# Kernel optimization log

Hardware: AMD Instinct MI355X
Metric: run time of the kernel (lower is better)

Reference implementation:

```python
import jax, jax.numpy as jnp
import numpy as np

NUM_HEADS = 8
NUM_GROUPS = 32
EPS = 1e-5


def setup_inputs() -> dict:
    key = jax.random.key(0)
    ks = jax.random.split(key, 7)
    B, C, H, W = 16, 512, 32, 32
    x = jax.random.normal(ks[0], (B, C, H, W), dtype=jnp.float32)
    gn_gamma = jnp.ones((C,), dtype=jnp.float32)
    gn_beta = jnp.zeros((C,), dtype=jnp.float32)
    # Conv1d with kernel_size=1 is a per-position matmul: weight [out, in]
    qkv_w = jax.random.normal(ks[1], (3 * C, C), dtype=jnp.float32) / np.sqrt(C)
    qkv_b = jax.random.normal(ks[2], (3 * C,), dtype=jnp.float32) * 0.01
    proj_w = jax.random.normal(ks[3], (C, C), dtype=jnp.float32) / np.sqrt(C)
    proj_b = jax.random.normal(ks[4], (C,), dtype=jnp.float32) * 0.01
    return {"x": x, "gn_gamma": gn_gamma, "gn_beta": gn_beta,
            "qkv_w": qkv_w, "qkv_b": qkv_b, "proj_w": proj_w, "proj_b": proj_b}


def group_norm(x, gamma, beta):
    # x: [B, C, H, W]
    B, C, H, W = x.shape
    xg = x.reshape(B, NUM_GROUPS, C // NUM_GROUPS, H, W)
    mean = xg.mean(axis=(2, 3, 4), keepdims=True)
    var = xg.var(axis=(2, 3, 4), keepdims=True)
    xg = (xg - mean) * jax.lax.rsqrt(var + EPS)
    x = xg.reshape(B, C, H, W)
    return x * gamma[None, :, None, None] + beta[None, :, None, None]


def reference(x, gn_gamma, gn_beta, qkv_w, qkv_b, proj_w, proj_b):
    B, C, H, W = x.shape
    N = H * W
    hd = C // NUM_HEADS  # head dim
    h = group_norm(x, gn_gamma, gn_beta).reshape(B, C, N)
    # 1x1 Conv1d == matmul over channel dim
    qkv = jnp.einsum('oc,bcn->bon', qkv_w, h) + qkv_b[None, :, None]
    qkv = qkv.reshape(B, 3, NUM_HEADS, hd, N)
    q, k, v = qkv[:, 0], qkv[:, 1], qkv[:, 2]  # each [B, h, d, N]
    scale = hd ** (-0.5)
    attn = jnp.einsum('bhdn,bhdm->bhnm', q, k) * scale  # [B, h, N, N]
    attn = jax.nn.softmax(attn, axis=-1)
    out = jnp.einsum('bhnm,bhdm->bhdn', attn, v).reshape(B, C, N)
    out = jnp.einsum('oc,bcn->bon', proj_w, out) + proj_b[None, :, None]
    return x + out.reshape(B, C, H, W)
```

## Files before the change

### kernel.cpp

```cpp
#include <hip/hip_runtime.h>

typedef unsigned short u16;
typedef unsigned int u32;
typedef __bf16 bf16x8 __attribute__((ext_vector_type(8)));
typedef float f32x4 __attribute__((ext_vector_type(4)));
typedef float f32x16 __attribute__((ext_vector_type(16)));

#define B_ 16
#define C_ 512
#define N_ 1024
#define NB_ 16384
#define K_ 512
#define M3_ 1536
#define SCALE_Q 0.18033688011112042f

__device__ __forceinline__ u16 f2bf(float f) {
  u32 u = __float_as_uint(f);
  u32 r = (u + 0x7FFFu + ((u >> 16) & 1u)) >> 16;
  return (u16)r;
}

__device__ __forceinline__ void gl_lds16(const void* g, void* l) {
  __builtin_amdgcn_global_load_lds(
      (const __attribute__((address_space(1))) u32*)(uintptr_t)g,
      (__attribute__((address_space(3))) u32*)(u32)(uintptr_t)l, 16, 0, 0);
}

__device__ __forceinline__ u32 cvtpk(float lo, float hi) {
  u32 r;
  asm("v_cvt_pk_bf16_f32 %0, %1, %2" : "=v"(r) : "v"(lo), "v"(hi));
  return r;
}

__device__ __forceinline__ float exp2a(float x) {
  float r;
  asm("v_exp_f32 %0, %1" : "=v"(r) : "v"(x));
  return r;
}

__device__ __forceinline__ void plswap2(u32& a, u32& b) {
#if __has_builtin(__builtin_amdgcn_permlane32_swap)
  auto r = __builtin_amdgcn_permlane32_swap((int)a, (int)b, false, false);
  a = (u32)r[0];
  b = (u32)r[1];
#else
  asm("v_permlane32_swap_b32 %0, %1" : "+v"(a), "+v"(b));
#endif
}

__device__ __forceinline__ float xhalf_sum(float x) {
  u32 a = __float_as_uint(x), b = a;
  plswap2(a, b);
  return __uint_as_float(a) + __uint_as_float(b);
}

__global__ __launch_bounds__(256) void cast_bf16_kernel(const float* __restrict__ src,
                                                        u16* __restrict__ dst, int n) {
  int i = blockIdx.x * 256 + threadIdx.x;
  if (i < n) dst[i] = f2bf(src[i]);
}

__global__ __launch_bounds__(256) void gnorm_kernel(const float* __restrict__ x,
                                                    const float* __restrict__ gamma,
                                                    const float* __restrict__ beta,
                                                    u16* __restrict__ ht) {
  int blk = blockIdx.x;
  int b = blk >> 5, g = blk & 31;
  int t = threadIdx.x;
  const float* xb = x + ((size_t)(b * C_ + g * 16) << 10);
  float v[16][4];
  float s = 0.f, sq = 0.f;
#pragma unroll
  for (int cc = 0; cc < 16; ++cc) {
#pragma unroll
    for (int r = 0; r < 4; ++r) {
      float f = xb[cc * 1024 + r * 256 + t];
      v[cc][r] = f; s += f; sq += f * f;
    }
  }
#pragma unroll
  for (int m = 32; m >= 1; m >>= 1) { s += __shfl_xor(s, m, 64); sq += __shfl_xor(sq, m, 64); }
  __shared__ float red[8];
  int w = t >> 6;
  if ((t & 63) == 0) { red[w * 2] = s; red[w * 2 + 1] = sq; }
  __syncthreads();
  s = red[0] + red[2] + red[4] + red[6];
  sq = red[1] + red[3] + red[5] + red[7];
  float mean = s * (1.f / 16384.f);
  float var = sq * (1.f / 16384.f) - mean * mean;
  float rstd = rsqrtf(var + 1e-5f);
  float gm[16], bt[16];
#pragma unroll
  for (int cc = 0; cc < 16; ++cc) {
    gm[cc] = gamma[g * 16 + cc] * rstd;
    bt[cc] = beta[g * 16 + cc];
  }
  u16* hb = ht + ((size_t)(b << 10)) * C_ + g * 16;
#pragma unroll
  for (int r = 0; r < 4; ++r) {
    u32 pk[8];
#pragma unroll
    for (int q = 0; q < 8; ++q) {
      float f0 = (v[2 * q][r] - mean) * gm[2 * q] + bt[2 * q];
      float f1 = (v[2 * q + 1][r] - mean) * gm[2 * q + 1] + bt[2 * q + 1];
      pk[q] = (u32)f2bf(f0) | ((u32)f2bf(f1) << 16);
    }
    u16* dp = hb + (size_t)(r * 256 + t) * C_;
    uint4 a = {pk[0], pk[1], pk[2], pk[3]};
    uint4 b4 = {pk[4], pk[5], pk[6], pk[7]};
    *(uint4*)dp = a;
    *(uint4*)(dp + 8) = b4;
  }
}

template <int EPI>
__global__ __launch_bounds__(256) void gemm_kernel(const u16* __restrict__ A,
                                                   const u16* __restrict__ BT,
                                                   const float* __restrict__ bias,
                                                   u16* __restrict__ Co,
                                                   u16* __restrict__ qTo,
                                                   u16* __restrict__ kTo,
                                                   const float* __restrict__ xres,
                                                   float* __restrict__ Fo) {
  __shared__ u16 ldsA[128 * 64];
  __shared__ u16 ldsB[128 * 64];
  int t = threadIdx.x;
  int l = t & 63, w = t >> 6;
  int wr = w >> 1, wc = w & 1;
  int ro0 = blockIdx.y * 128, co0 = blockIdx.x * 128;
  f32x4 acc[4][4];
#pragma unroll
  for (int m = 0; m < 4; ++m)
#pragma unroll
    for (int n = 0; n < 4; ++n) acc[m][n] = {0.f, 0.f, 0.f, 0.f};
  int srow = t >> 3, sg = t & 7;
  for (int kt = 0; kt < 8; ++kt) {
    int k0 = kt * 64;
#pragma unroll
    for (int i = 0; i < 4; ++i) {
      int row = i * 32 + srow;
      int gl = sg ^ (row & 7);
      gl_lds16(A + (size_t)(ro0 + row) * K_ + k0 + gl * 8, ldsA + (i * 32 + w * 8) * 64);
      gl_lds16(BT + (size_t)(co0 + row) * K_ + k0 + gl * 8, ldsB + (i * 32 + w * 8) * 64);
    }
    __syncthreads();
#pragma unroll
    for (int ks = 0; ks < 2; ++ks) {
      bf16x8 af[4], bfr[4];
#pragma unroll
      for (int m = 0; m < 4; ++m) {
        int row = wr * 64 + m * 16 + (l & 15);
        int ph = (ks * 4 + (l >> 4)) ^ (row & 7);
        af[m] = *(const bf16x8*)&ldsA[row * 64 + ph * 8];
      }
#pragma unroll
      for (int n = 0; n < 4; ++n) {
        int row = wc * 64 + n * 16 + (l & 15);
        int ph = (ks * 4 + (l >> 4)) ^ (row & 7);
        bfr[n] = *(const bf16x8*)&ldsB[row * 64 + ph * 8];
      }
#pragma unroll
      for (int m = 0; m < 4; ++m)
#pragma unroll
        for (int n = 0; n < 4; ++n)
          acc[m][n] = __builtin_amdgcn_mfma_f32_16x16x32_bf16(af[m], bfr[n], acc[m][n], 0, 0, 0);
    }
    __syncthreads();
  }
  if (EPI == 0 && ro0 < 1024) {
    int sel = ro0 >> 9;
    u16* dstb = sel ? kTo : qTo;
    float scl = sel ? 1.f : SCALE_Q;
#pragma unroll
    for (int m = 0; m < 4; ++m) {
      int row0 = ro0 + wr * 64 + m * 16 + (l >> 4) * 4;
      int o = row0 & 511;
      int h = o >> 6, d0 = o & 63;
      float bv0 = bias[row0], bv1 = bias[row0 + 1];
      float bv2 = bias[row0 + 2], bv3 = bias[row0 + 3];
#pragma unroll
      for (int n = 0; n < 4; ++n) {
        int col = co0 + wc * 64 + n * 16 + (l & 15);
        int bb = col >> 10, nn = col & 1023;
        float v0 = (acc[m][n][0] + bv0) * scl;
        float v1 = (acc[m][n][1] + bv1) * scl;
        float v2 = (acc[m][n][2] + bv2) * scl;
        float v3 = (acc[m][n][3] + bv3) * scl;
        uint2 ov = {cvtpk(v0, v1), cvtpk(v2, v3)};
        *(uint2*)(dstb + ((size_t)((bb * 8 + h) << 10) + nn) * 64 + d0) = ov;
      }
    }
  } else {
#pragma unroll
    for (int m = 0; m < 4; ++m) {
#pragma unroll
      for (int j = 0; j < 4; ++j) {
        int row = ro0 + wr * 64 + m * 16 + (l >> 4) * 4 + j;
        float bv = bias[row];
#pragma unroll
        for (int n = 0; n < 4; ++n) {
          int col = co0 + wc * 64 + n * 16 + (l & 15);
          float val = acc[m][n][j] + bv;
          if (EPI == 0) {
            Co[(size_t)row * NB_ + col] = f2bf(val);
          } else {
            int bb = col >> 10, nn = col & 1023;
            size_t oi = (((size_t)(bb * C_ + row)) << 10) + nn;
            Fo[oi] = xres[oi] + val;
          }
        }
      }
    }
  }
}

__global__ __launch_bounds__(128) void attn_kernel(const u16* __restrict__ qT,
                                                   const u16* __restrict__ kT,
                                                   const u16* __restrict__ qkv,
                                                   u16* __restrict__ aoT) {
  __shared__ u16 Kall[2][2][2048];
  __shared__ u16 Vall[2][2][2048];
  int bid = blockIdx.x;
  int wid = (bid & 7) * 128 + (bid >> 3);
  int qt2 = wid & 7, h = (wid >> 3) & 7, b = wid >> 6;
  int bh = b * 8 + h;
  int t = threadIdx.x, l = t & 63, w = t >> 6;
  int lq = l & 31, hi = l >> 5;
  int q0 = qt2 * 128 + w * 64;

  u16* Kw = &Kall[w][0][0];
  u16* Vw = &Vall[w][0][0];

  bf16x8 qf[2][4];
#pragma unroll
  for (int qg = 0; qg < 2; ++qg) {
    const u16* qbase = qT + ((size_t)(bh << 10) + q0 + qg * 32 + lq) * 64 + hi * 8;
#pragma unroll
    for (int kc = 0; kc < 4; ++kc) qf[qg][kc] = *(const bf16x8*)(qbase + kc * 16);
  }

  f32x16 accO[2][2];
#pragma unroll
  for (int qg = 0; qg < 2; ++qg)
#pragma unroll
    for (int dt = 0; dt < 2; ++dt)
#pragma unroll
      for (int r = 0; r < 16; ++r) accO[qg][dt][r] = 0.f;
  float lsum[2] = {0.f, 0.f};

  const u16* k_src = kT + ((size_t)(bh << 10) + (l >> 3)) * 64 + (((l & 7) ^ ((l >> 3) & 7)) * 8);
  const u16* v_src = qkv + (size_t)(2 * C_ + h * 64 + (l >> 2)) * NB_ + (b << 10) +
                     (((l & 3) ^ ((l >> 3) & 3)) * 8);

  const u16* kfp[4];
#pragma unroll
  for (int kc = 0; kc < 4; ++kc)
    kfp[kc] = Kw + lq * 64 + (((2 * kc + hi) ^ (lq & 7)) * 8);
  const u16* vfp[4];
#pragma unroll
  for (int dt = 0; dt < 2; ++dt)
#pragma unroll
    for (int kcc = 0; kcc < 2; ++kcc)
      vfp[dt * 2 + kcc] = Vw + (dt * 32 + lq) * 32 + (((kcc * 2 + hi) ^ ((lq >> 1) & 3)) * 8);

  auto stage = [&](int buf) {
    u16* Kd = Kw + buf * 2048;
    u16* Vd = Vw + buf * 2048;
#pragma unroll
    for (int i = 0; i < 4; ++i) gl_lds16(k_src + i * 512, Kd + i * 512);
#pragma unroll
    for (int i = 0; i < 4; ++i) gl_lds16(v_src + (size_t)i * 16 * NB_, Vd + i * 512);
    k_src += 2048;
    v_src += 32;
  };

  auto step = [&](int buf, bool dostage) {
    if (dostage) {
      stage(buf ^ 1);
      asm volatile("s_waitcnt vmcnt(8)" ::: "memory");
    } else {
      asm volatile("s_waitcnt vmcnt(0)" ::: "memory");
    }
    __builtin_amdgcn_sched_barrier(0);
    bf16x8 kf[4], vf[4];
#pragma unroll
    for (int kc = 0; kc < 4; ++kc) kf[kc] = *(const bf16x8*)(kfp[kc] + buf * 2048);
#pragma unroll
    for (int j = 0; j < 4; ++j) vf[j] = *(const bf16x8*)(vfp[j] + buf * 2048);
    f32x16 sc[2];
#pragma unroll
    for (int qg = 0; qg < 2; ++qg)
#pragma unroll
      for (int r = 0; r < 16; ++r) sc[qg][r] = 0.f;
    __builtin_amdgcn_s_setprio(1);
#pragma unroll
    for (int kc = 0; kc < 4; ++kc) {
      sc[0] = __builtin_amdgcn_mfma_f32_32x32x16_bf16(kf[kc], qf[0][kc], sc[0], 0, 0, 0);
      sc[1] = __builtin_amdgcn_mfma_f32_32x32x16_bf16(kf[kc], qf[1][kc], sc[1], 0, 0, 0);
    }
    __builtin_amdgcn_s_setprio(0);
    u32 pfu[2][2][4];
#pragma unroll
    for (int qg = 0; qg < 2; ++qg) {
      float ps = 0.f;
#pragma unroll
      for (int r = 0; r < 16; ++r) {
        float e = exp2a(sc[qg][r]);
        sc[qg][r] = e;
        ps += e;
      }
      lsum[qg] += ps;
      u32 pk[8];
#pragma unroll
      for (int p = 0; p < 8; ++p) pk[p] = cvtpk(sc[qg][2 * p], sc[qg][2 * p + 1]);
#pragma unroll
      for (int cc = 0; cc < 2; ++cc) {
        u32 w0 = pk[cc * 4 + 0], w2 = pk[cc * 4 + 2];
        u32 w1 = pk[cc * 4 + 1], w3 = pk[cc * 4 + 3];
        plswap2(w0, w2);
        plswap2(w1, w3);
        pfu[qg][cc][0] = w0; pfu[qg][cc][1] = w1;
        pfu[qg][cc][2] = w2; pfu[qg][cc][3] = w3;
      }
    }
    __builtin_amdgcn_s_setprio(1);
#pragma unroll
    for (int kcc = 0; kcc < 2; ++kcc)
#pragma unroll
      for (int dt = 0; dt < 2; ++dt) {
        bf16x8 vv = vf[dt * 2 + kcc];
#pragma unroll
        for (int qg = 0; qg < 2; ++qg) {
          union { u32 u[4]; bf16x8 v; } pf;
          pf.u[0] = pfu[qg][kcc][0]; pf.u[1] = pfu[qg][kcc][1];
          pf.u[2] = pfu[qg][kcc][2]; pf.u[3] = pfu[qg][kcc][3];
          accO[qg][dt] = __builtin_amdgcn_mfma_f32_32x32x16_bf16(vv, pf.v, accO[qg][dt], 0, 0, 0);
        }
      }
    __builtin_amdgcn_s_setprio(0);
  };

  stage(0);
#pragma unroll 1
  for (int s = 0; s < 15; ++s) {
    step(0, true);
    step(1, true);
  }
  step(0, true);
  step(1, false);

#pragma unroll
  for (int qg = 0; qg < 2; ++qg) {
    float inv = 1.0f / xhalf_sum(lsum[qg]);
    u16* ob = aoT + ((size_t)((b << 10) + q0 + qg * 32 + lq)) * C_ + h * 64;
#pragma unroll
    for (int dt = 0; dt < 2; ++dt)
#pragma unroll
      for (int rg = 0; rg < 4; ++rg) {
        int d0 = dt * 32 + rg * 8 + hi * 4;
        u32 w0 = cvtpk(accO[qg][dt][rg * 4 + 0] * inv, accO[qg][dt][rg * 4 + 1] * inv);
        u32 w1 = cvtpk(accO[qg][dt][rg * 4 + 2] * inv, accO[qg][dt][rg * 4 + 3] * inv);
        uint2 o = {w0, w1};
        *(uint2*)(ob + d0) = o;
      }
  }
}

extern "C" void kernel_launch(void* const* d_in, const int* in_sizes, int n_in,
                              void* d_out, int out_size, void* d_ws, size_t ws_size,
                              hipStream_t stream) {
  const float* x = (const float*)d_in[0];
  const float* gamma = (const float*)d_in[1];
  const float* beta = (const float*)d_in[2];
  const float* qkv_w = (const float*)d_in[3];
  const float* qkv_b = (const float*)d_in[4];
  const float* proj_w = (const float*)d_in[5];
  const float* proj_b = (const float*)d_in[6];
  float* out = (float*)d_out;
  char* ws = (char*)d_ws;
  u16* wq = (u16*)(ws);
  u16* wp = (u16*)(ws + 1572864);
  u16* ht = (u16*)(ws + 2097152);
  u16* qkvo = (u16*)(ws + 18874368);
  u16* qT = (u16*)(ws + 69206016);
  u16* kT = (u16*)(ws + 85983232);
  u16* aoT = ht;

  cast_bf16_kernel<<<3072, 256, 0, stream>>>(qkv_w, wq, M3_ * K_);
  cast_bf16_kernel<<<1024, 256, 0, stream>>>(proj_w, wp, C_ * K_);
  gnorm_kernel<<<512, 256, 0, stream>>>(x, gamma, beta, ht);
  gemm_kernel<0><<<dim3(128, 12), 256, 0, stream>>>(wq, ht, qkv_b, qkvo, qT, kT, nullptr, nullptr);
  attn_kernel<<<1024, 128, 0, stream>>>(qT, kT, qkvo, aoT);
  gemm_kernel<1><<<dim3(128, 4), 256, 0, stream>>>(wp, aoT, proj_b, nullptr, nullptr, nullptr, x, out);
}
```

Measured before the change: 135.4 us.

## Split attention KV range across wave pairs with LDS reduction of partial outputs

The attention block grows from 2 to 4 waves. Each pair of query waves now splits the 1024 keys in half, so the serial loop is 16 steps instead of 32. K and V tiles are shared through LDS, with one wave loading K and the other loading V, synchronised by block barriers. At the end, the partial output accumulators and row sums are combined through LDS before normalising. This adds barriers and a final reduction in exchange for more parallelism per block, and it also splits the exp-sum accumulation into four independent chains.

Measured after the change: 379.3 us. 2.8x slower.

```diff
diff --git a/kernel.cpp b/kernel.cpp
--- a/kernel.cpp
+++ b/kernel.cpp
@@ -214,22 +214,20 @@
   }
 }
 
-__global__ __launch_bounds__(128) void attn_kernel(const u16* __restrict__ qT,
-                                                   const u16* __restrict__ kT,
-                                                   const u16* __restrict__ qkv,
-                                                   u16* __restrict__ aoT) {
-  __shared__ u16 Kall[2][2][2048];
-  __shared__ u16 Vall[2][2][2048];
+__global__ __launch_bounds__(256, 4) void attn_kernel(const u16* __restrict__ qT,
+                                                      const u16* __restrict__ kT,
+                                                      const u16* __restrict__ qkv,
+                                                      u16* __restrict__ aoT) {
+  __shared__ u16 KV[2][2][4096];
+  __shared__ float smL[2][2][64];
   int bid = blockIdx.x;
   int wid = (bid & 7) * 128 + (bid >> 3);
   int qt2 = wid & 7, h = (wid >> 3) & 7, b = wid >> 6;
   int bh = b * 8 + h;
   int t = threadIdx.x, l = t & 63, w = t >> 6;
+  int wq = w >> 1, wk = w & 1;
   int lq = l & 31, hi = l >> 5;
-  int q0 = qt2 * 128 + w * 64;
-
-  u16* Kw = &Kall[w][0][0];
-  u16* Vw = &Vall[w][0][0];
+  int q0 = qt2 * 128 + wq * 64;
 
   bf16x8 qf[2][4];
 #pragma unroll
@@ -248,45 +246,48 @@
       for (int r = 0; r < 16; ++r) accO[qg][dt][r] = 0.f;
   float lsum[2] = {0.f, 0.f};
 
-  const u16* k_src = kT + ((size_t)(bh << 10) + (l >> 3)) * 64 + (((l & 7) ^ ((l >> 3) & 7)) * 8);
-  const u16* v_src = qkv + (size_t)(2 * C_ + h * 64 + (l >> 2)) * NB_ + (b << 10) +
+  const u16* k_src = kT + ((size_t)(bh << 10) + wk * 512 + (l >> 3)) * 64 +
+                     (((l & 7) ^ ((l >> 3) & 7)) * 8);
+  const u16* v_src = qkv + (size_t)(2 * C_ + h * 64 + (l >> 2)) * NB_ + (b << 10) + wk * 512 +
                      (((l & 3) ^ ((l >> 3) & 3)) * 8);
 
+  u16* kvbase = &KV[wk][0][0];
+
   const u16* kfp[4];
 #pragma unroll
   for (int kc = 0; kc < 4; ++kc)
-    kfp[kc] = Kw + lq * 64 + (((2 * kc + hi) ^ (lq & 7)) * 8);
+    kfp[kc] = kvbase + lq * 64 + (((2 * kc + hi) ^ (lq & 7)) * 8);
   const u16* vfp[4];
 #pragma unroll
   for (int dt = 0; dt < 2; ++dt)
 #pragma unroll
     for (int kcc = 0; kcc < 2; ++kcc)
-      vfp[dt * 2 + kcc] = Vw + (dt * 32 + lq) * 32 + (((kcc * 2 + hi) ^ ((lq >> 1) & 3)) * 8);
+      vfp[dt * 2 + kcc] = kvbase + 2048 + (dt * 32 + lq) * 32 + (((kcc * 2 + hi) ^ ((lq >> 1) & 3)) * 8);
 
   auto stage = [&](int buf) {
-    u16* Kd = Kw + buf * 2048;
-    u16* Vd = Vw + buf * 2048;
-#pragma unroll
-    for (int i = 0; i < 4; ++i) gl_lds16(k_src + i * 512, Kd + i * 512);
-#pragma unroll
-    for (int i = 0; i < 4; ++i) gl_lds16(v_src + (size_t)i * 16 * NB_, Vd + i * 512);
-    k_src += 2048;
-    v_src += 32;
+    u16* dst = kvbase + buf * 4096 + (wq ? 2048 : 0);
+    if (wq == 0) {
+#pragma unroll
+      for (int i = 0; i < 4; ++i) gl_lds16(k_src + i * 512, dst + i * 512);
+      k_src += 2048;
+    } else {
+#pragma unroll
+      for (int i = 0; i < 4; ++i) gl_lds16(v_src + (size_t)i * 16 * NB_, dst + i * 512);
+      v_src += 32;
+    }
   };
 
   auto step = [&](int buf, bool dostage) {
-    if (dostage) {
-      stage(buf ^ 1);
-      asm volatile("s_waitcnt vmcnt(8)" ::: "memory");
-    } else {
-      asm volatile("s_waitcnt vmcnt(0)" ::: "memory");
-    }
+    asm volatile("s_waitcnt vmcnt(0)" ::: "memory");
     __builtin_amdgcn_sched_barrier(0);
+    __builtin_amdgcn_s_barrier();
+    __builtin_amdgcn_sched_barrier(0);
+    if (dostage) stage(buf ^ 1);
     bf16x8 kf[4], vf[4];
 #pragma unroll
-    for (int kc = 0; kc < 4; ++kc) kf[kc] = *(const bf16x8*)(kfp[kc] + buf * 2048);
-#pragma unroll
-    for (int j = 0; j < 4; ++j) vf[j] = *(const bf16x8*)(vfp[j] + buf * 2048);
+    for (int kc = 0; kc < 4; ++kc) kf[kc] = *(const bf16x8*)(kfp[kc] + buf * 4096);
+#pragma unroll
+    for (int j = 0; j < 4; ++j) vf[j] = *(const bf16x8*)(vfp[j] + buf * 4096);
     f32x16 sc[2];
 #pragma unroll
     for (int qg = 0; qg < 2; ++qg)
@@ -302,14 +303,18 @@
     u32 pfu[2][2][4];
 #pragma unroll
     for (int qg = 0; qg < 2; ++qg) {
-      float ps = 0.f;
-#pragma unroll
-      for (int r = 0; r < 16; ++r) {
-        float e = exp2a(sc[qg][r]);
-        sc[qg][r] = e;
-        ps += e;
-      }
-      lsum[qg] += ps;
+      float p0 = 0.f, p1 = 0.f, p2 = 0.f, p3 = 0.f;
+#pragma unroll
+      for (int r = 0; r < 4; ++r) {
+        float e0 = exp2a(sc[qg][4 * r + 0]);
+        float e1 = exp2a(sc[qg][4 * r + 1]);
+        float e2 = exp2a(sc[qg][4 * r + 2]);
+        float e3 = exp2a(sc[qg][4 * r + 3]);
+        sc[qg][4 * r + 0] = e0; sc[qg][4 * r + 1] = e1;
+        sc[qg][4 * r + 2] = e2; sc[qg][4 * r + 3] = e3;
+        p0 += e0; p1 += e1; p2 += e2; p3 += e3;
+      }
+      lsum[qg] += (p0 + p1) + (p2 + p3);
       u32 pk[8];
 #pragma unroll
       for (int p = 0; p < 8; ++p) pk[p] = cvtpk(sc[qg][2 * p], sc[qg][2 * p + 1]);
@@ -342,27 +347,49 @@
 
   stage(0);
 #pragma unroll 1
-  for (int s = 0; s < 15; ++s) {
+  for (int s = 0; s < 7; ++s) {
     step(0, true);
     step(1, true);
   }
   step(0, true);
   step(1, false);
 
-#pragma unroll
-  for (int qg = 0; qg < 2; ++qg) {
-    float inv = 1.0f / xhalf_sum(lsum[qg]);
-    u16* ob = aoT + ((size_t)((b << 10) + q0 + qg * 32 + lq)) * C_ + h * 64;
-#pragma unroll
-    for (int dt = 0; dt < 2; ++dt)
-#pragma unroll
-      for (int rg = 0; rg < 4; ++rg) {
-        int d0 = dt * 32 + rg * 8 + hi * 4;
-        u32 w0 = cvtpk(accO[qg][dt][rg * 4 + 0] * inv, accO[qg][dt][rg * 4 + 1] * inv);
-        u32 w1 = cvtpk(accO[qg][dt][rg * 4 + 2] * inv, accO[qg][dt][rg * 4 + 3] * inv);
-        uint2 o = {w0, w1};
-        *(uint2*)(ob + d0) = o;
-      }
+  __syncthreads();
+  float* mb = (float*)&KV[0][0][0];
+  if (wk == 1) {
+#pragma unroll
+    for (int qg = 0; qg < 2; ++qg) {
+      smL[wq][qg][l] = lsum[qg];
+#pragma unroll
+      for (int dt = 0; dt < 2; ++dt)
+#pragma unroll
+        for (int r = 0; r < 16; ++r)
+          mb[wq * 4096 + (qg * 32 + dt * 16 + r) * 64 + l] = accO[qg][dt][r];
+    }
+  }
+  __syncthreads();
+  if (wk == 0) {
+#pragma unroll
+    for (int qg = 0; qg < 2; ++qg) {
+      lsum[qg] += smL[wq][qg][l];
+#pragma unroll
+      for (int dt = 0; dt < 2; ++dt)
+#pragma unroll
+        for (int r = 0; r < 16; ++r)
+          accO[qg][dt][r] += mb[wq * 4096 + (qg * 32 + dt * 16 + r) * 64 + l];
+      float inv = 1.0f / xhalf_sum(lsum[qg]);
+      u16* ob = aoT + ((size_t)((b << 10) + q0 + qg * 32 + lq)) * C_ + h * 64;
+#pragma unroll
+      for (int dt = 0; dt < 2; ++dt)
+#pragma unroll
+        for (int rg = 0; rg < 4; ++rg) {
+          int d0 = dt * 32 + rg * 8 + hi * 4;
+          u32 w0 = cvtpk(accO[qg][dt][rg * 4 + 0] * inv, accO[qg][dt][rg * 4 + 1] * inv);
+          u32 w1 = cvtpk(accO[qg][dt][rg * 4 + 2] * inv, accO[qg][dt][rg * 4 + 3] * inv);
+          uint2 o = {w0, w1};
+          *(uint2*)(ob + d0) = o;
+        }
+    }
   }
 }
 
@@ -390,6 +417,6 @@
   cast_bf16_kernel<<<1024, 256, 0, stream>>>(proj_w, wp, C_ * K_);
   gnorm_kernel<<<512, 256, 0, stream>>>(x, gamma, beta, ht);
   gemm_kernel<0><<<dim3(128, 12), 256, 0, stream>>>(wq, ht, qkv_b, qkvo, qT, kT, nullptr, nullptr);
-  attn_kernel<<<1024, 128, 0, stream>>>(qT, kT, qkvo, aoT);
+  attn_kernel<<<1024, 256, 0, stream>>>(qT, kT, qkvo, aoT);
   gemm_kernel<1><<<dim3(128, 4), 256, 0, stream>>>(wp, aoT, proj_b, nullptr, nullptr, nullptr, x, out);
 }
```

## Share K/V tiles across four waves per block with cooperative staging

Applied to the files above, without the earlier changes.

The attention kernel goes from 2 waves per block, each handling 64 queries with private K/V LDS buffers, to 4 waves per block, each handling 32 queries and sharing one double-buffered K/V tile. Each wave now issues only two global-to-LDS loads per step (two waves load K, two load V), so global and LDS traffic per query tile drops and per-wave register pressure falls. In exchange, every step now needs a full vmcnt(0) wait plus a workgroup barrier, and each wave has half the MFMA work available to hide latency. The exp2 sum is also split into four partial accumulators.

New measurement: 131.3 us. 3.0% less time.

```diff
diff --git a/kernel.cpp b/kernel.cpp
--- a/kernel.cpp
+++ b/kernel.cpp
@@ -214,128 +214,122 @@
   }
 }
 
-__global__ __launch_bounds__(128) void attn_kernel(const u16* __restrict__ qT,
+__global__ __launch_bounds__(256) void attn_kernel(const u16* __restrict__ qT,
                                                    const u16* __restrict__ kT,
                                                    const u16* __restrict__ qkv,
                                                    u16* __restrict__ aoT) {
-  __shared__ u16 Kall[2][2][2048];
-  __shared__ u16 Vall[2][2][2048];
+  __shared__ u16 KV[2][4096];
   int bid = blockIdx.x;
   int wid = (bid & 7) * 128 + (bid >> 3);
   int qt2 = wid & 7, h = (wid >> 3) & 7, b = wid >> 6;
   int bh = b * 8 + h;
   int t = threadIdx.x, l = t & 63, w = t >> 6;
   int lq = l & 31, hi = l >> 5;
-  int q0 = qt2 * 128 + w * 64;
-
-  u16* Kw = &Kall[w][0][0];
-  u16* Vw = &Vall[w][0][0];
-
-  bf16x8 qf[2][4];
-#pragma unroll
-  for (int qg = 0; qg < 2; ++qg) {
-    const u16* qbase = qT + ((size_t)(bh << 10) + q0 + qg * 32 + lq) * 64 + hi * 8;
-#pragma unroll
-    for (int kc = 0; kc < 4; ++kc) qf[qg][kc] = *(const bf16x8*)(qbase + kc * 16);
-  }
-
-  f32x16 accO[2][2];
-#pragma unroll
-  for (int qg = 0; qg < 2; ++qg)
-#pragma unroll
-    for (int dt = 0; dt < 2; ++dt)
-#pragma unroll
-      for (int r = 0; r < 16; ++r) accO[qg][dt][r] = 0.f;
-  float lsum[2] = {0.f, 0.f};
-
-  const u16* k_src = kT + ((size_t)(bh << 10) + (l >> 3)) * 64 + (((l & 7) ^ ((l >> 3) & 7)) * 8);
-  const u16* v_src = qkv + (size_t)(2 * C_ + h * 64 + (l >> 2)) * NB_ + (b << 10) +
-                     (((l & 3) ^ ((l >> 3) & 3)) * 8);
+  int q0 = qt2 * 128 + w * 32;
+
+  const u16* qbase = qT + ((size_t)(bh << 10) + q0 + lq) * 64 + hi * 8;
+  bf16x8 qf[4];
+#pragma unroll
+  for (int kc = 0; kc < 4; ++kc) qf[kc] = *(const bf16x8*)(qbase + kc * 16);
+
+  f32x16 accO[2];
+#pragma unroll
+  for (int dt = 0; dt < 2; ++dt)
+#pragma unroll
+    for (int r = 0; r < 16; ++r) accO[dt][r] = 0.f;
+  float lsum = 0.f;
+
+  const u16 *src0, *src1;
+  u32 ldso0, ldso1;
+  int adv;
+  if (w < 2) {
+    int i0 = 2 * w, i1 = 2 * w + 1;
+    src0 = kT + ((size_t)(bh << 10) + i0 * 8 + (l >> 3)) * 64 + (((l & 7) ^ ((l >> 3) & 7)) * 8);
+    src1 = kT + ((size_t)(bh << 10) + i1 * 8 + (l >> 3)) * 64 + (((l & 7) ^ ((l >> 3) & 7)) * 8);
+    ldso0 = i0 * 512; ldso1 = i1 * 512;
+    adv = 2048;
+  } else {
+    int j0 = 2 * (w - 2), j1 = 2 * (w - 2) + 1;
+    src0 = qkv + (size_t)(2 * C_ + h * 64 + j0 * 16 + (l >> 2)) * NB_ + (b << 10) +
+           (((l & 3) ^ ((l >> 3) & 3)) * 8);
+    src1 = qkv + (size_t)(2 * C_ + h * 64 + j1 * 16 + (l >> 2)) * NB_ + (b << 10) +
+           (((l & 3) ^ ((l >> 3) & 3)) * 8);
+    ldso0 = 2048 + j0 * 512; ldso1 = 2048 + j1 * 512;
+    adv = 32;
+  }
 
   const u16* kfp[4];
 #pragma unroll
   for (int kc = 0; kc < 4; ++kc)
-    kfp[kc] = Kw + lq * 64 + (((2 * kc + hi) ^ (lq & 7)) * 8);
+    kfp[kc] = &KV[0][0] + lq * 64 + (((2 * kc + hi) ^ (lq & 7)) * 8);
   const u16* vfp[4];
 #pragma unroll
   for (int dt = 0; dt < 2; ++dt)
 #pragma unroll
     for (int kcc = 0; kcc < 2; ++kcc)
-      vfp[dt * 2 + kcc] = Vw + (dt * 32 + lq) * 32 + (((kcc * 2 + hi) ^ ((lq >> 1) & 3)) * 8);
+      vfp[dt * 2 + kcc] = &KV[0][0] + 2048 + (dt * 32 + lq) * 32 +
+                          (((kcc * 2 + hi) ^ ((lq >> 1) & 3)) * 8);
 
   auto stage = [&](int buf) {
-    u16* Kd = Kw + buf * 2048;
-    u16* Vd = Vw + buf * 2048;
-#pragma unroll
-    for (int i = 0; i < 4; ++i) gl_lds16(k_src + i * 512, Kd + i * 512);
-#pragma unroll
-    for (int i = 0; i < 4; ++i) gl_lds16(v_src + (size_t)i * 16 * NB_, Vd + i * 512);
-    k_src += 2048;
-    v_src += 32;
+    gl_lds16(src0, &KV[buf][0] + ldso0);
+    gl_lds16(src1, &KV[buf][0] + ldso1);
+    src0 += adv;
+    src1 += adv;
   };
 
   auto step = [&](int buf, bool dostage) {
-    if (dostage) {
-      stage(buf ^ 1);
-      asm volatile("s_waitcnt vmcnt(8)" ::: "memory");
-    } else {
-      asm volatile("s_waitcnt vmcnt(0)" ::: "memory");
-    }
+    asm volatile("s_waitcnt vmcnt(0)" ::: "memory");
     __builtin_amdgcn_sched_barrier(0);
-    bf16x8 kf[4], vf[4];
-#pragma unroll
-    for (int kc = 0; kc < 4; ++kc) kf[kc] = *(const bf16x8*)(kfp[kc] + buf * 2048);
-#pragma unroll
-    for (int j = 0; j < 4; ++j) vf[j] = *(const bf16x8*)(vfp[j] + buf * 2048);
-    f32x16 sc[2];
-#pragma unroll
-    for (int qg = 0; qg < 2; ++qg)
-#pragma unroll
-      for (int r = 0; r < 16; ++r) sc[qg][r] = 0.f;
+    __builtin_amdgcn_s_barrier();
+    __builtin_amdgcn_sched_barrier(0);
+    if (dostage) stage(buf ^ 1);
+    bf16x8 kf[4];
+#pragma unroll
+    for (int kc = 0; kc < 4; ++kc) kf[kc] = *(const bf16x8*)(kfp[kc] + buf * 4096);
+    f32x16 sc;
+#pragma unroll
+    for (int r = 0; r < 16; ++r) sc[r] = 0.f;
     __builtin_amdgcn_s_setprio(1);
 #pragma unroll
-    for (int kc = 0; kc < 4; ++kc) {
-      sc[0] = __builtin_amdgcn_mfma_f32_32x32x16_bf16(kf[kc], qf[0][kc], sc[0], 0, 0, 0);
-      sc[1] = __builtin_amdgcn_mfma_f32_32x32x16_bf16(kf[kc], qf[1][kc], sc[1], 0, 0, 0);
-    }
+    for (int kc = 0; kc < 4; ++kc)
+      sc = __builtin_amdgcn_mfma_f32_32x32x16_bf16(kf[kc], qf[kc], sc, 0, 0, 0);
     __builtin_amdgcn_s_setprio(0);
-    u32 pfu[2][2][4];
-#pragma unroll
-    for (int qg = 0; qg < 2; ++qg) {
-      float ps = 0.f;
-#pragma unroll
-      for (int r = 0; r < 16; ++r) {
-        float e = exp2a(sc[qg][r]);
-        sc[qg][r] = e;
-        ps += e;
-      }
-      lsum[qg] += ps;
-      u32 pk[8];
-#pragma unroll
-      for (int p = 0; p < 8; ++p) pk[p] = cvtpk(sc[qg][2 * p], sc[qg][2 * p + 1]);
-#pragma unroll
-      for (int cc = 0; cc < 2; ++cc) {
-        u32 w0 = pk[cc * 4 + 0], w2 = pk[cc * 4 + 2];
-        u32 w1 = pk[cc * 4 + 1], w3 = pk[cc * 4 + 3];
-        plswap2(w0, w2);
-        plswap2(w1, w3);
-        pfu[qg][cc][0] = w0; pfu[qg][cc][1] = w1;
-        pfu[qg][cc][2] = w2; pfu[qg][cc][3] = w3;
-      }
+    bf16x8 vf[4];
+#pragma unroll
+    for (int j = 0; j < 4; ++j) vf[j] = *(const bf16x8*)(vfp[j] + buf * 4096);
+    float p0 = 0.f, p1 = 0.f, p2 = 0.f, p3 = 0.f;
+#pragma unroll
+    for (int r = 0; r < 4; ++r) {
+      float e0 = exp2a(sc[4 * r + 0]);
+      float e1 = exp2a(sc[4 * r + 1]);
+      float e2 = exp2a(sc[4 * r + 2]);
+      float e3 = exp2a(sc[4 * r + 3]);
+      sc[4 * r + 0] = e0; sc[4 * r + 1] = e1;
+      sc[4 * r + 2] = e2; sc[4 * r + 3] = e3;
+      p0 += e0; p1 += e1; p2 += e2; p3 += e3;
+    }
+    lsum += (p0 + p1) + (p2 + p3);
+    u32 pk[8];
+#pragma unroll
+    for (int p = 0; p < 8; ++p) pk[p] = cvtpk(sc[2 * p], sc[2 * p + 1]);
+    u32 pfu[2][4];
+#pragma unroll
+    for (int cc = 0; cc < 2; ++cc) {
+      u32 w0 = pk[cc * 4 + 0], w2 = pk[cc * 4 + 2];
+      u32 w1 = pk[cc * 4 + 1], w3 = pk[cc * 4 + 3];
+      plswap2(w0, w2);
+      plswap2(w1, w3);
+      pfu[cc][0] = w0; pfu[cc][1] = w1; pfu[cc][2] = w2; pfu[cc][3] = w3;
     }
     __builtin_amdgcn_s_setprio(1);
 #pragma unroll
     for (int kcc = 0; kcc < 2; ++kcc)
 #pragma unroll
       for (int dt = 0; dt < 2; ++dt) {
-        bf16x8 vv = vf[dt * 2 + kcc];
-#pragma unroll
-        for (int qg = 0; qg < 2; ++qg) {
-          union { u32 u[4]; bf16x8 v; } pf;
-          pf.u[0] = pfu[qg][kcc][0]; pf.u[1] = pfu[qg][kcc][1];
-          pf.u[2] = pfu[qg][kcc][2]; pf.u[3] = pfu[qg][kcc][3];
-          accO[qg][dt] = __builtin_amdgcn_mfma_f32_32x32x16_bf16(vv, pf.v, accO[qg][dt], 0, 0, 0);
-        }
+        union { u32 u[4]; bf16x8 v; } pf;
+        pf.u[0] = pfu[kcc][0]; pf.u[1] = pfu[kcc][1];
+        pf.u[2] = pfu[kcc][2]; pf.u[3] = pfu[kcc][3];
+        accO[dt] = __builtin_amdgcn_mfma_f32_32x32x16_bf16(vf[dt * 2 + kcc], pf.v, accO[dt], 0, 0, 0);
       }
     __builtin_amdgcn_s_setprio(0);
   };
@@ -349,21 +343,18 @@
   step(0, true);
   step(1, false);
 
-#pragma unroll
-  for (int qg = 0; qg < 2; ++qg) {
-    float inv = 1.0f / xhalf_sum(lsum[qg]);
-    u16* ob = aoT + ((size_t)((b << 10) + q0 + qg * 32 + lq)) * C_ + h * 64;
-#pragma unroll
-    for (int dt = 0; dt < 2; ++dt)
-#pragma unroll
-      for (int rg = 0; rg < 4; ++rg) {
-        int d0 = dt * 32 + rg * 8 + hi * 4;
-        u32 w0 = cvtpk(accO[qg][dt][rg * 4 + 0] * inv, accO[qg][dt][rg * 4 + 1] * inv);
-        u32 w1 = cvtpk(accO[qg][dt][rg * 4 + 2] * inv, accO[qg][dt][rg * 4 + 3] * inv);
-        uint2 o = {w0, w1};
-        *(uint2*)(ob + d0) = o;
-      }
-  }
+  float inv = 1.0f / xhalf_sum(lsum);
+  u16* ob = aoT + ((size_t)((b << 10) + q0 + lq)) * C_ + h * 64;
+#pragma unroll
+  for (int dt = 0; dt < 2; ++dt)
+#pragma unroll
+    for (int rg = 0; rg < 4; ++rg) {
+      int d0 = dt * 32 + rg * 8 + hi * 4;
+      u32 w0 = cvtpk(accO[dt][rg * 4 + 0] * inv, accO[dt][rg * 4 + 1] * inv);
+      u32 w1 = cvtpk(accO[dt][rg * 4 + 2] * inv, accO[dt][rg * 4 + 3] * inv);
+      uint2 o = {w0, w1};
+      *(uint2*)(ob + d0) = o;
+    }
 }
 
 extern "C" void kernel_launch(void* const* d_in, const int* in_sizes, int n_in,
@@ -390,6 +381,6 @@
   cast_bf16_kernel<<<1024, 256, 0, stream>>>(proj_w, wp, C_ * K_);
   gnorm_kernel<<<512, 256, 0, stream>>>(x, gamma, beta, ht);
   gemm_kernel<0><<<dim3(128, 12), 256, 0, stream>>>(wq, ht, qkv_b, qkvo, qT, kT, nullptr, nullptr);
-  attn_kernel<<<1024, 128, 0, stream>>>(qT, kT, qkvo, aoT);
+  attn_kernel<<<1024, 256, 0, stream>>>(qT, kT, qkvo, aoT);
   gemm_kernel<1><<<dim3(128, 4), 256, 0, stream>>>(wp, aoT, proj_b, nullptr, nullptr, nullptr, x, out);
 }
```
